# Kernel optimization log

Measured on AMD Instinct MI355X. Metric: run time of the kernel, lower is better.

Reference implementation:

```python
import jax, jax.numpy as jnp
import numpy as np
from math import lgamma

# dims (match init_kwargs / input_specs)
N_MELS = 80; MEM_DIM = 256; PRE1 = 256; PRE2 = 128
ATTN_LSTM = 256; ATTN_DIM = 128; S_FILT = 8; S_K = 21; D_FILT = 8; D_K = 21
P_LEN = 11; ALPHA = 0.1; BETA = 0.9; DEC_LSTM = 256; R = 2
B = 32; T_MELS = 400; T_ENC = 200


def _betabinom_prior():
    # beta-binomial pmf over [0, P_LEN-1] with n = P_LEN-1, a=ALPHA, b=BETA
    n = P_LEN - 1
    def pmf(k):
        return np.exp(lgamma(n + 1) - lgamma(k + 1) - lgamma(n - k + 1)
                      + lgamma(k + ALPHA) + lgamma(n - k + BETA) - lgamma(n + ALPHA + BETA)
                      - (lgamma(ALPHA) + lgamma(BETA) - lgamma(ALPHA + BETA)))
    return np.array([pmf(k) for k in range(P_LEN)], dtype=np.float32)


def setup_inputs() -> dict:
    ks = iter(jax.random.split(jax.random.key(0), 40))
    def w(*shape):
        return jax.random.normal(next(ks), shape, jnp.float32) / float(np.sqrt(shape[-1]))
    inp = {}
    inp["mels"] = jax.random.normal(next(ks), (B, N_MELS, T_MELS), jnp.float32)
    inp["memory"] = jax.random.normal(next(ks), (B, T_ENC, MEM_DIM), jnp.float32)
    # prenet
    inp["pre_W1"] = w(PRE1, N_MELS); inp["pre_b1"] = jnp.zeros((PRE1,), jnp.float32)
    inp["pre_W2"] = w(PRE2, PRE1); inp["pre_b2"] = jnp.zeros((PRE2,), jnp.float32)
    # attention LSTMCell (input = prenet[-1] + memory_dim)
    inp["al_Wih"] = w(4 * ATTN_LSTM, PRE2 + MEM_DIM); inp["al_Whh"] = w(4 * ATTN_LSTM, ATTN_LSTM)
    inp["al_bih"] = jnp.zeros((4 * ATTN_LSTM,), jnp.float32); inp["al_bhh"] = jnp.zeros((4 * ATTN_LSTM,), jnp.float32)
    # dynamic convolution attention
    inp["att_W"] = w(ATTN_DIM, ATTN_LSTM); inp["att_Wb"] = jnp.zeros((ATTN_DIM,), jnp.float32)
    inp["att_V"] = w(D_FILT * D_K, ATTN_DIM)
    inp["att_F"] = w(S_FILT, 1, S_K)
    inp["att_U"] = w(ATTN_DIM, S_FILT)
    inp["att_T"] = w(ATTN_DIM, D_FILT); inp["att_Tb"] = jnp.zeros((ATTN_DIM,), jnp.float32)
    inp["att_v"] = w(ATTN_DIM)
    inp["prior"] = jnp.asarray(_betabinom_prior())
    # decoder LSTMCell (input = attn_lstm_size + memory_dim)
    inp["dl_Wih"] = w(4 * DEC_LSTM, ATTN_LSTM + MEM_DIM); inp["dl_Whh"] = w(4 * DEC_LSTM, DEC_LSTM)
    inp["dl_bih"] = jnp.zeros((4 * DEC_LSTM,), jnp.float32); inp["dl_bhh"] = jnp.zeros((4 * DEC_LSTM,), jnp.float32)
    # acoustic projection
    inp["ac_W"] = w(N_MELS * R, DEC_LSTM + MEM_DIM); inp["ac_b"] = jnp.zeros((N_MELS * R,), jnp.float32)
    return inp


def _forward(mels, memory, pre_W1, pre_b1, pre_W2, pre_b2,
             al_Wih, al_Whh, al_bih, al_bhh,
             att_W, att_Wb, att_V, att_F, att_U, att_T, att_Tb, att_v, prior,
             dl_Wih, dl_Whh, dl_bih, dl_bhh, ac_W, ac_b):
    Bq = mels.shape[0]
    dn = ('NCH', 'OIH', 'NCH')
    prior_k = prior[::-1][None, None, :]  # torch registers flipped prior as conv kernel

    def lstm(x, h, c, Wih, Whh, bih, bhh):
        gates = x @ Wih.T + bih + h @ Whh.T + bhh
        i, f, g, o = jnp.split(gates, 4, axis=-1)
        c_new = jax.nn.sigmoid(f) * c + jax.nn.sigmoid(i) * jnp.tanh(g)
        return jax.nn.sigmoid(o) * jnp.tanh(c_new), c_new

    def dca(query, align):
        # query [B, attn_lstm], align [B, T_enc]
        T = align.shape[-1]
        # causal prior convolution, log-clamped
        p = jax.lax.conv_general_dilated(align[:, None, :], prior_k, (1,), [(P_LEN - 1, 0)], dimension_numbers=dn)[:, 0]
        p = jnp.log(jnp.clip(p, 1e-6))
        # per-example dynamic filters G: [B, C*K]
        G = jnp.tanh(query @ att_W.T + att_Wb) @ att_V.T
        g = jax.lax.conv_general_dilated(align[None, :, :], G.reshape(Bq * D_FILT, 1, D_K), (1,),
                                         [((D_K - 1) // 2,) * 2], dimension_numbers=dn,
                                         feature_group_count=Bq)[0].reshape(Bq, D_FILT, T)
        # static filters: [B, S, T]
        f = jax.lax.conv_general_dilated(align[:, None, :], att_F, (1,), [((S_K - 1) // 2,) * 2], dimension_numbers=dn)
        e = jnp.tanh(jnp.einsum('bst,as->bta', f, att_U) + jnp.einsum('bct,ac->bta', g, att_T) + att_Tb) @ att_v
        return jax.nn.softmax(e + p, axis=-1)

    def step(carry, x):
        align, ctx, h1, c1, h2, c2 = carry
        # prenet (dropout disabled: eval-mode deterministic reference)
        pre = jax.nn.relu(jax.nn.relu(x @ pre_W1.T + pre_b1) @ pre_W2.T + pre_b2)
        h1, c1 = lstm(jnp.concatenate([ctx, pre], -1), h1, c1, al_Wih, al_Whh, al_bih, al_bhh)
        align = dca(h1, align)
        ctx = jnp.einsum('bt,btd->bd', align, memory)
        h2, c2 = lstm(jnp.concatenate([h1, ctx], -1), h2, c2, dl_Wih, dl_Whh, dl_bih, dl_bhh)
        out = (jnp.concatenate([h2, ctx], -1) @ ac_W.T + ac_b).reshape(Bq, N_MELS, R)
        return (align, ctx, h1, c1, h2, c2), (out, align)

    T_enc = memory.shape[1]
    align0 = jnp.zeros((Bq, T_enc), jnp.float32).at[:, 0].set(1.0)  # one-hot at position 0
    carry0 = (align0,
              jnp.zeros((Bq, MEM_DIM), jnp.float32),
              jnp.zeros((Bq, ATTN_LSTM), jnp.float32), jnp.zeros((Bq, ATTN_LSTM), jnp.float32),
              jnp.zeros((Bq, DEC_LSTM), jnp.float32), jnp.zeros((Bq, DEC_LSTM), jnp.float32))
    # teacher forcing: step t>0 consumes ground-truth frame mels[:, :, t-1] for t in range(0, T, R)
    frames = jnp.moveaxis(mels[:, :, R - 1::R], 2, 0)  # [steps, B, N]
    xs = jnp.concatenate([jnp.zeros((1, Bq, N_MELS), jnp.float32), frames[:-1]], axis=0)
    _, (outs, aligns) = jax.lax.scan(step, carry0, xs)
    output_mels = jnp.moveaxis(outs, 0, 2).reshape(Bq, N_MELS, -1)  # cat along time: [B, N, T]
    alignments = jnp.moveaxis(aligns, 0, 2)  # stack dim=2: [B, T_enc, steps]
    return output_mels, alignments


def reference(mels, memory, pre_W1, pre_b1, pre_W2, pre_b2,
              al_Wih, al_Whh, al_bih, al_bhh,
              att_W, att_Wb, att_V, att_F, att_U, att_T, att_Tb, att_v, prior,
              dl_Wih, dl_Whh, dl_bih, dl_bhh, ac_W, ac_b):
    return _forward(mels, memory, pre_W1, pre_b1, pre_W2, pre_b2,
                    al_Wih, al_Whh, al_bih, al_bhh,
                    att_W, att_Wb, att_V, att_F, att_U, att_T, att_Tb, att_v, prior,
                    dl_Wih, dl_Whh, dl_bih, dl_bhh, ac_W, ac_b)
```

## Files before the change

kernel.cpp:

```cpp
#include <hip/hip_runtime.h>
#include <math.h>

#define BB 32
#define TENC 200
#define NMELS 80
#define TMELS 400
#define STEPS 200
#define MEM 256
#define PRE1N 256
#define PRE2N 128
#define AD 128
#define DK 21
#define DF 8
#define SK 21
#define SF 8
#define PL 11
#define BLK 1024

#define QW1 0u
#define QW2 655360u
#define HP5 1441792u
#define WS_ATTWT 761856u
#define WS_PW1T  816128u
#define WS_PW2T  836608u
#define WS_PRE2  869376u
#define WS_MEMH  1688576u
#define WS_AVTH  2507776u

#define L_XS   0
#define L_H1   768
#define L_C1   1024
#define L_H2   1280
#define L_C2   1536
#define L_CTX  1792
#define L_AL   2048
#define L_PS   2248
#define L_ES   2448
#define L_P4   2656
#define L_QS   6752
#define L_GS   6880
#define L_FS   7048
#define L_WF   8648
#define L_PR   8816
#define L_RB   8828
#define L_B1   8848
#define L_B2   9872
#define L_AW   10896
#define DYNF   27280
#define DYNB   (DYNF*4)

__device__ __forceinline__ float sigm(float x){ return 1.f/(1.f+__expf(-x)); }
__device__ __forceinline__ float tanh_fast(float x){
  float ax = fabsf(x);
  float z = __expf(-2.f*ax);
  float r = (1.f - z)/(1.f + z);
  return (x < 0.f) ? -r : r;
}
__device__ __forceinline__ unsigned short to_bf16(float f){
  unsigned u = __float_as_uint(f);
  return (unsigned short)((u + 0x7fffu + ((u>>16)&1u)) >> 16);
}

#define FMA8S(wv, xa, xb, acc) \
  acc += __uint_as_float((wv).x<<16)*(xa).x + __uint_as_float((wv).x&0xffff0000u)*(xa).y \
       + __uint_as_float((wv).y<<16)*(xa).z + __uint_as_float((wv).y&0xffff0000u)*(xa).w \
       + __uint_as_float((wv).z<<16)*(xb).x + __uint_as_float((wv).z&0xffff0000u)*(xb).y \
       + __uint_as_float((wv).w<<16)*(xb).z + __uint_as_float((wv).w&0xffff0000u)*(xb).w;

__global__ __launch_bounds__(256) void trk(const float* __restrict__ s, float* __restrict__ d, int R, int C){
  int i = blockIdx.x*256 + threadIdx.x;
  if (i < R*C){ int r = i / C, c = i - r*C; d[c*R + r] = s[i]; }
}
__global__ __launch_bounds__(256) void pkq1c(const float* __restrict__ wih, const float* __restrict__ whh,
                                             unsigned short* __restrict__ d){
  int i = blockIdx.x*256 + threadIdx.x;
  if (i < 1024*640){
    int c = i / 640, k = i - c*640;
    float v = (k < 384) ? wih[c*384 + k] : whh[c*256 + (k-384)];
    int q = k / 160, kr = k - 160*q, kk = kr >> 3, e = kr & 7;
    d[((unsigned)((q*20 + kk)*1024 + c))*8u + e] = to_bf16(v);
  }
}
__global__ __launch_bounds__(256) void pkq2c(const float* __restrict__ wih, const float* __restrict__ whh,
                                             unsigned short* __restrict__ d){
  int i = blockIdx.x*256 + threadIdx.x;
  if (i < 1024*768){
    int c = i / 768, k = i - c*768;
    float v = (k < 512) ? wih[c*512 + k] : whh[c*256 + (k-512)];
    int q = k / 192, kr = k - 192*q, kk = kr >> 3, e = kr & 7;
    d[((unsigned)((q*24 + kk)*1024 + c))*8u + e] = to_bf16(v);
  }
}
__global__ __launch_bounds__(256) void pk8h(const float* __restrict__ s, unsigned short* __restrict__ d, int R, int C){
  int i = blockIdx.x*256 + threadIdx.x;
  if (i < R*C){ int r = i / C, c = i - r*C; d[(unsigned)(c>>3)*(unsigned)R*8u + (unsigned)r*8u + (c&7)] = to_bf16(s[i]); }
}
__global__ __launch_bounds__(256) void pkmem(const float* __restrict__ s, unsigned short* __restrict__ d, int n){
  int i = blockIdx.x*256 + threadIdx.x;
  if (i < n) d[i] = to_bf16(s[i]);
}
__global__ __launch_bounds__(256) void pkavt(const float* __restrict__ s, unsigned short* __restrict__ d){
  int i = blockIdx.x*256 + threadIdx.x;
  if (i < 128*168){ int k = i/168, a = i - k*168; d[i] = to_bf16(s[a*128 + k]); }
}

__global__ __launch_bounds__(256) void prenetk(const float* __restrict__ mels,
    const float* __restrict__ b1, const float* __restrict__ b2, float* __restrict__ ws){
  int t = blockIdx.x, tid = threadIdx.x;
  __shared__ float xS[BB*NMELS];
  __shared__ float p1S[BB*PRE1N];
  const float* W1T = ws + WS_PW1T;
  const float* W2T = ws + WS_PW2T;
  for (int i=tid;i<BB*NMELS;i+=256){
    int r = i/NMELS, k = i - r*NMELS;
    xS[i] = (t==0)?0.f : mels[r*NMELS*TMELS + k*TMELS + (2*t-1)];
  }
  __syncthreads();
  {
    float acc[BB];
    #pragma unroll
    for (int r=0;r<BB;r++) acc[r]=0.f;
    for (int k=0;k<NMELS;k++){
      float w = W1T[k*PRE1N + tid];
      #pragma unroll
      for (int r=0;r<BB;r++) acc[r] += xS[r*NMELS+k]*w;
    }
    float bb = b1[tid];
    #pragma unroll
    for (int r=0;r<BB;r++) p1S[r*PRE1N+tid] = fmaxf(acc[r]+bb, 0.f);
  }
  __syncthreads();
  if (tid < PRE2N){
    float acc[BB];
    #pragma unroll
    for (int r=0;r<BB;r++) acc[r]=0.f;
    for (int k=0;k<PRE1N;k++){
      float w = W2T[k*PRE2N + tid];
      #pragma unroll
      for (int r=0;r<BB;r++) acc[r] += p1S[r*PRE1N+k]*w;
    }
    float bb = b2[tid];
    #pragma unroll
    for (int r=0;r<BB;r++) ws[WS_PRE2 + ((unsigned)t*BB + r)*PRE2N + tid] = fmaxf(acc[r]+bb, 0.f);
  }
}

__global__ __launch_bounds__(BLK) void decoder(
    const float* __restrict__ albih, const float* __restrict__ albhh,
    const float* __restrict__ dlbih, const float* __restrict__ dlbhh,
    const float* __restrict__ prior, const float* __restrict__ attF,
    const float* __restrict__ attWb, const float* __restrict__ attU,
    const float* __restrict__ attT, const float* __restrict__ attTb,
    const float* __restrict__ attv,
    const float* __restrict__ acb, const float* __restrict__ ws,
    float* __restrict__ out){
  extern __shared__ float sm[];
  const int b = blockIdx.x, tid = threadIdx.x;
  unsigned short* aWh = (unsigned short*)(sm + L_AW);
  const unsigned* aWu = (const unsigned*)(sm + L_AW);

  if (tid < 256){
    sm[L_H1+tid]=0.f; sm[L_C1+tid]=0.f; sm[L_H2+tid]=0.f; sm[L_C2+tid]=0.f; sm[L_CTX+tid]=0.f;
    sm[L_XS+tid]=0.f;
    sm[L_XS+384+tid]=0.f;
  }
  if (tid >= 256 && tid < 384) sm[L_XS+tid] = ws[WS_PRE2 + ((unsigned)0*BB + b)*PRE2N + (tid-256)];
  if (tid < TENC) sm[L_AL+tid] = (tid==0)?1.f:0.f;
  sm[L_B1+tid] = albih[tid] + albhh[tid];
  sm[L_B2+tid] = dlbih[tid] + dlbhh[tid];
  if (tid < SF*SK) sm[L_WF+tid] = attF[tid];
  if (tid < PL)    sm[L_PR+tid] = prior[tid];
  for (int i = tid; i < 32768; i += BLK) aWh[i] = to_bf16(ws[WS_ATTWT + i]);
  __syncthreads();

  const unsigned short* hw = (const unsigned short*)ws;
  const unsigned short* Q1 = hw + QW1;
  const unsigned short* Q2 = hw + QW2;
  const unsigned short* P5 = hw + HP5;
  const unsigned* memh = (const unsigned*)(ws + WS_MEMH);
  const unsigned short* avth = (const unsigned short*)(ws + WS_AVTH);
  const int q = tid >> 8, c0 = tid & 255;

  for (int t = 0; t < STEPS; ++t){
    {
      const float* xq = sm + L_XS + 160*q;
      const unsigned short* Wq = Q1 + (unsigned)q*163840u;
      float a0=0.f, a1=0.f, a2=0.f, a3=0.f;
      #pragma unroll 2
      for (int kk = 0; kk < 20; kk++){
        float4 xa = *(const float4*)(xq + 8*kk);
        float4 xb = *(const float4*)(xq + 8*kk + 4);
        const unsigned short* wr = Wq + (unsigned)kk*8192u + c0*8u;
        uint4 w0 = *(const uint4*)(wr);
        uint4 w1 = *(const uint4*)(wr + 2048);
        uint4 w2 = *(const uint4*)(wr + 4096);
        uint4 w3 = *(const uint4*)(wr + 6144);
        FMA8S(w0, xa, xb, a0)
        FMA8S(w1, xa, xb, a1)
        FMA8S(w2, xa, xb, a2)
        FMA8S(w3, xa, xb, a3)
      }
      sm[L_P4 + q*1024 + c0      ] = a0;
      sm[L_P4 + q*1024 + c0 + 256] = a1;
      sm[L_P4 + q*1024 + c0 + 512] = a2;
      sm[L_P4 + q*1024 + c0 + 768] = a3;
    }
    __syncthreads();
    if (tid < 256){
      float g[4];
      #pragma unroll
      for (int gg2 = 0; gg2 < 4; gg2++){
        int col = gg2*256 + tid;
        g[gg2] = sm[L_B1+col] + sm[L_P4+col] + sm[L_P4+1024+col] + sm[L_P4+2048+col] + sm[L_P4+3072+col];
      }
      float c = sigm(g[1])*sm[L_C1+tid] + sigm(g[0])*tanh_fast(g[2]);
      sm[L_C1+tid] = c;
      sm[L_H1+tid] = sigm(g[3])*tanh_fast(c);
    }
    __syncthreads();
    if (tid < 512){
      const int quarter = tid >> 7, a = tid & 127;
      const int sel = a & 1, au = a >> 1;
      float s = 0.f;
      for (int k = 64*quarter; k < 64*quarter+64; k++){
        unsigned u = aWu[k*64 + au];
        float wv = __uint_as_float(sel ? (u & 0xffff0000u) : (u << 16));
        s += sm[L_H1+k]*wv;
      }
      sm[L_P4 + tid] = s;
    } else if (tid < 512+TENC){
      const int pos = tid - 512;
      float s = 0.f;
      #pragma unroll
      for (int jj = 0; jj < PL; jj++){ int qq = pos - jj; if (qq >= 0) s += sm[L_PR+jj]*sm[L_AL+qq]; }
      sm[L_PS+pos] = __logf(fmaxf(s, 1e-6f));
      #pragma unroll
      for (int c = 0; c < SF; c++){
        float s2 = 0.f;
        #pragma unroll
        for (int k = 0; k < SK; k++){ int qq = pos + k - 10; if (qq>=0 && qq<TENC) s2 += sm[L_WF+c*SK+k]*sm[L_AL+qq]; }
        sm[L_FS + c*TENC + pos] = s2;
      }
    } else if (tid < 872){
      if (t >= 1){
        const int col = tid - 712;
        float a0=0.f, a1=0.f;
        #pragma unroll 2
        for (int kk = 0; kk < 64; kk += 2){
          const float* xp0 = (kk   < 32) ? (sm + L_H2 + 8*kk)     : (sm + L_CTX + 8*kk - 256);
          const float* xp1 = (kk+1 < 32) ? (sm + L_H2 + 8*(kk+1)) : (sm + L_CTX + 8*(kk+1) - 256);
          uint4 w0 = *(const uint4*)(P5 + (unsigned)(kk  )*1280u + col*8u);
          uint4 w1 = *(const uint4*)(P5 + (unsigned)(kk+1)*1280u + col*8u);
          FMA8S(w0, *(const float4*)xp0, *(const float4*)(xp0+4), a0)
          FMA8S(w1, *(const float4*)xp1, *(const float4*)(xp1+4), a1)
        }
        const int m = col >> 1, r = col & 1;
        out[(unsigned)b*NMELS*TMELS + m*TMELS + 2*(t-1) + r] = a0+a1 + acb[col];
      }
    }
    __syncthreads();
    if (tid < AD) sm[L_QS+tid] = tanh_fast(attWb[tid] + sm[L_P4+tid] + sm[L_P4+128+tid] + sm[L_P4+256+tid] + sm[L_P4+384+tid]);
    __syncthreads();
    if (tid < DF*DK){
      float a = 0.f;
      for (int k = 0; k < AD; k++) a += sm[L_QS+k]*__uint_as_float(((unsigned)avth[k*(DF*DK)+tid])<<16);
      sm[L_GS+tid] = a;
    }
    __syncthreads();
    if (tid < 4*TENC){
      const int pos = tid >> 2, qr = tid & 3;
      float g[DF];
      #pragma unroll
      for (int c=0;c<DF;c++){
        float s=0.f;
        #pragma unroll
        for (int k=0;k<DK;k++){
          int q2 = pos + k - 10;
          if (q2>=0 && q2<TENC) s += sm[L_AL+q2]*sm[L_GS+c*DK+k];
        }
        g[c]=s;
      }
      float fv[SF];
      #pragma unroll
      for (int s2=0;s2<SF;s2++) fv[s2] = sm[L_FS + s2*TENC + pos];
      float pp = 0.f;
      for (int h = qr*32; h < qr*32+32; h++){
        float u = attTb[h];
        #pragma unroll
        for (int s2=0;s2<SF;s2++) u += attU[h*SF+s2]*fv[s2];
        #pragma unroll
        for (int c=0;c<DF;c++) u += attT[h*DF+c]*g[c];
        pp += attv[h]*tanh_fast(u);
      }
      pp += __shfl_xor(pp,1);
      pp += __shfl_xor(pp,2);
      if (qr==0) sm[L_ES+pos] = pp + sm[L_PS+pos];
    }
    __syncthreads();
    if (tid < 64){
      float v0 = sm[L_ES+tid], v1 = sm[L_ES+64+tid], v2 = sm[L_ES+128+tid];
      float v3 = (tid < 8) ? sm[L_ES+192+tid] : -3.0e38f;
      float mx = fmaxf(fmaxf(v0,v1), fmaxf(v2,v3));
      for (int o=1;o<64;o<<=1) mx = fmaxf(mx, __shfl_xor(mx,o));
      float e0 = __expf(v0-mx), e1 = __expf(v1-mx), e2 = __expf(v2-mx);
      float e3 = (tid < 8) ? __expf(v3-mx) : 0.f;
      float sv = ((e0+e1)+(e2+e3));
      for (int o=1;o<64;o<<=1) sv += __shfl_xor(sv,o);
      float inv = 1.f/sv;
      float a0 = e0*inv, a1 = e1*inv, a2 = e2*inv;
      sm[L_AL+tid] = a0; sm[L_AL+64+tid] = a1; sm[L_AL+128+tid] = a2;
      unsigned ob = 1024000u + (unsigned)b*TENC*STEPS + (unsigned)t;
      out[ob + (unsigned)tid*STEPS]       = a0;
      out[ob + (unsigned)(64+tid)*STEPS]  = a1;
      out[ob + (unsigned)(128+tid)*STEPS] = a2;
      if (tid < 8){
        float a3 = e3*inv;
        sm[L_AL+192+tid] = a3;
        out[ob + (unsigned)(192+tid)*STEPS] = a3;
      }
    }
    __syncthreads();
    {
      const int grp2 = tid >> 7, jp = tid & 127;
      const unsigned base = ((unsigned)b*TENC)*128u + jp;
      float a0 = 0.f, a1 = 0.f;
      for (int p = grp2*25; p < grp2*25+25; p++){
        unsigned u = memh[base + (unsigned)p*128u];
        float al = sm[L_AL+p];
        a0 += al*__uint_as_float(u << 16);
        a1 += al*__uint_as_float(u & 0xffff0000u);
      }
      sm[L_P4 + grp2*256 + 2*jp    ] = a0;
      sm[L_P4 + grp2*256 + 2*jp + 1] = a1;
    }
    __syncthreads();
    if (tid < 256){
      float c = 0.f;
      #pragma unroll
      for (int g2 = 0; g2 < 8; g2++) c += sm[L_P4 + g2*256 + tid];
      sm[L_CTX+tid] = c;
      sm[L_XS+256+tid] = c;
    } else if (tid < 512){
      sm[L_XS + (tid-256)] = sm[L_H1 + (tid-256)];
    } else if (tid < 768){
      sm[L_XS + tid] = sm[L_H2 + (tid-512)];
    }
    __syncthreads();
    {
      const float* xq = sm + L_XS + 192*q;
      const unsigned short* Wq = Q2 + (unsigned)q*196608u;
      float a0=0.f, a1=0.f, a2=0.f, a3=0.f;
      #pragma unroll 2
      for (int kk = 0; kk < 24; kk++){
        float4 xa = *(const float4*)(xq + 8*kk);
        float4 xb = *(const float4*)(xq + 8*kk + 4);
        const unsigned short* wr = Wq + (unsigned)kk*8192u + c0*8u;
        uint4 w0 = *(const uint4*)(wr);
        uint4 w1 = *(const uint4*)(wr + 2048);
        uint4 w2 = *(const uint4*)(wr + 4096);
        uint4 w3 = *(const uint4*)(wr + 6144);
        FMA8S(w0, xa, xb, a0)
        FMA8S(w1, xa, xb, a1)
        FMA8S(w2, xa, xb, a2)
        FMA8S(w3, xa, xb, a3)
      }
      sm[L_P4 + q*1024 + c0      ] = a0;
      sm[L_P4 + q*1024 + c0 + 256] = a1;
      sm[L_P4 + q*1024 + c0 + 512] = a2;
      sm[L_P4 + q*1024 + c0 + 768] = a3;
    }
    __syncthreads();
    if (tid < 256){
      float g[4];
      #pragma unroll
      for (int gg2 = 0; gg2 < 4; gg2++){
        int col = gg2*256 + tid;
        g[gg2] = sm[L_B2+col] + sm[L_P4+col] + sm[L_P4+1024+col] + sm[L_P4+2048+col] + sm[L_P4+3072+col];
      }
      float c = sigm(g[1])*sm[L_C2+tid] + sigm(g[0])*tanh_fast(g[2]);
      sm[L_C2+tid] = c;
      sm[L_H2+tid] = sigm(g[3])*tanh_fast(c);
    } else if (tid < 384){
      if (t+1 < STEPS)
        sm[L_XS+tid] = __builtin_nontemporal_load(&ws[WS_PRE2 + ((unsigned)(t+1)*BB + b)*PRE2N + (tid-256)]);
    } else if (tid < 640){
      sm[L_XS+tid] = sm[L_H1 + (tid-384)];
    } else if (tid < 896){
      sm[L_XS + (tid-640)] = sm[L_CTX + (tid-640)];
    }
    __syncthreads();
  }
  if (tid < 160){
    const int col = tid;
    float a0=0.f, a1=0.f;
    #pragma unroll 2
    for (int kk = 0; kk < 64; kk += 2){
      const float* xp0 = (kk   < 32) ? (sm + L_H2 + 8*kk)     : (sm + L_CTX + 8*kk - 256);
      const float* xp1 = (kk+1 < 32) ? (sm + L_H2 + 8*(kk+1)) : (sm + L_CTX + 8*(kk+1) - 256);
      uint4 w0 = *(const uint4*)(P5 + (unsigned)(kk  )*1280u + col*8u);
      uint4 w1 = *(const uint4*)(P5 + (unsigned)(kk+1)*1280u + col*8u);
      FMA8S(w0, *(const float4*)xp0, *(const float4*)(xp0+4), a0)
      FMA8S(w1, *(const float4*)xp1, *(const float4*)(xp1+4), a1)
    }
    const int m = col >> 1, r = col & 1;
    out[(unsigned)b*NMELS*TMELS + m*TMELS + 2*(STEPS-1) + r] = a0+a1 + acb[col];
  }
}

extern "C" void kernel_launch(void* const* d_in, const int* in_sizes, int n_in,
                              void* d_out, int out_size, void* d_ws, size_t ws_size,
                              hipStream_t stream) {
  (void)in_sizes; (void)n_in; (void)out_size; (void)ws_size;
  const float* mels   = (const float*)d_in[0];
  const float* memory = (const float*)d_in[1];
  const float* pre_W1 = (const float*)d_in[2];
  const float* pre_b1 = (const float*)d_in[3];
  const float* pre_W2 = (const float*)d_in[4];
  const float* pre_b2 = (const float*)d_in[5];
  const float* al_Wih = (const float*)d_in[6];
  const float* al_Whh = (const float*)d_in[7];
  const float* al_bih = (const float*)d_in[8];
  const float* al_bhh = (const float*)d_in[9];
  const float* att_W  = (const float*)d_in[10];
  const float* att_Wb = (const float*)d_in[11];
  const float* att_V  = (const float*)d_in[12];
  const float* att_F  = (const float*)d_in[13];
  const float* att_U  = (const float*)d_in[14];
  const float* att_T  = (const float*)d_in[15];
  const float* att_Tb = (const float*)d_in[16];
  const float* att_v  = (const float*)d_in[17];
  const float* prior  = (const float*)d_in[18];
  const float* dl_Wih = (const float*)d_in[19];
  const float* dl_Whh = (const float*)d_in[20];
  const float* dl_bih = (const float*)d_in[21];
  const float* dl_bhh = (const float*)d_in[22];
  const float* ac_W   = (const float*)d_in[23];
  const float* ac_b   = (const float*)d_in[24];
  float* ws  = (float*)d_ws;
  unsigned short* hw = (unsigned short*)d_ws;
  float* out = (float*)d_out;

  hipFuncSetAttribute((const void*)decoder, hipFuncAttributeMaxDynamicSharedMemorySize, DYNB);

  auto TR = [&](const float* src, unsigned off, int R, int C){
    int n = R*C;
    trk<<<dim3((n+255)/256), dim3(256), 0, stream>>>(src, ws + off, R, C);
  };
  pkq1c<<<dim3((1024*640+255)/256), dim3(256), 0, stream>>>(al_Wih, al_Whh, hw + QW1);
  pkq2c<<<dim3((1024*768+255)/256), dim3(256), 0, stream>>>(dl_Wih, dl_Whh, hw + QW2);
  pk8h<<<dim3((160*512+255)/256), dim3(256), 0, stream>>>(ac_W, hw + HP5, 160, 512);
  TR(att_W,  WS_ATTWT, 128, 256);
  TR(pre_W1, WS_PW1T,  256, 80);
  TR(pre_W2, WS_PW2T,  128, 256);
  {
    int n = BB*TENC*MEM;
    pkmem<<<dim3((n+255)/256), dim3(256), 0, stream>>>(memory, (unsigned short*)(ws + WS_MEMH), n);
  }
  pkavt<<<dim3((128*168+255)/256), dim3(256), 0, stream>>>(att_V, (unsigned short*)(ws + WS_AVTH));

  prenetk<<<dim3(STEPS), dim3(256), 0, stream>>>(mels, pre_b1, pre_b2, ws);

  decoder<<<dim3(BB), dim3(BLK), DYNB, stream>>>(
      al_bih, al_bhh, dl_bih, dl_bhh, prior, att_F,
      att_Wb, att_U, att_T, att_Tb, att_v,
      ac_b, ws, out);
}
```

Measured before the change: 23.50 ms.

## Switch decoder weights and activations to fp16 with packed dot2 instructions

Converts all packed weights and memory from bf16 to fp16. LSTM inputs, hidden states and context are now kept in shared memory as fp16 vectors, so the matvecs use v_dot2_f32_f16 instead of unpacking bf16 and doing scalar FMAs. The attention W matrix is repacked into padded rows of half2 pairs so the query projection is also dot2-based. The aim is to cut ALU work and shared-memory traffic per step. In exchange, fp16 has less range than bf16, and the activations are now quantized as well as the weights.

```diff
diff --git a/kernel.cpp b/kernel.cpp
--- a/kernel.cpp
+++ b/kernel.cpp
@@ -27,27 +27,28 @@
 #define WS_MEMH  1688576u
 #define WS_AVTH  2507776u
 
-#define L_XS   0
-#define L_H1   768
-#define L_C1   1024
-#define L_H2   1280
-#define L_C2   1536
-#define L_CTX  1792
-#define L_AL   2048
-#define L_PS   2248
-#define L_ES   2448
-#define L_P4   2656
-#define L_QS   6752
-#define L_GS   6880
-#define L_FS   7048
-#define L_WF   8648
-#define L_PR   8816
-#define L_RB   8828
-#define L_B1   8848
-#define L_B2   9872
-#define L_AW   10896
-#define DYNF   27280
+#define L_C1   0
+#define L_C2   256
+#define L_AL   512
+#define L_PS   712
+#define L_ES   912
+#define L_QS   1120
+#define L_GS   1248
+#define L_WF   1416
+#define L_PR   1584
+#define L_B1   1600
+#define L_B2   2624
+#define L_FS   3648
+#define L_P4   5248
+#define L_AW   9344
+#define L_XB1  25856
+#define L_XB2  26240
+#define L_H1B  26624
+#define L_H2B  26752
+#define DYNF   26880
 #define DYNB   (DYNF*4)
+
+typedef _Float16 h2v __attribute__((ext_vector_type(2)));
 
 __device__ __forceinline__ float sigm(float x){ return 1.f/(1.f+__expf(-x)); }
 __device__ __forceinline__ float tanh_fast(float x){
@@ -56,16 +57,21 @@
   float r = (1.f - z)/(1.f + z);
   return (x < 0.f) ? -r : r;
 }
-__device__ __forceinline__ unsigned short to_bf16(float f){
-  unsigned u = __float_as_uint(f);
-  return (unsigned short)((u + 0x7fffu + ((u>>16)&1u)) >> 16);
-}
-
-#define FMA8S(wv, xa, xb, acc) \
-  acc += __uint_as_float((wv).x<<16)*(xa).x + __uint_as_float((wv).x&0xffff0000u)*(xa).y \
-       + __uint_as_float((wv).y<<16)*(xa).z + __uint_as_float((wv).y&0xffff0000u)*(xa).w \
-       + __uint_as_float((wv).z<<16)*(xb).x + __uint_as_float((wv).z&0xffff0000u)*(xb).y \
-       + __uint_as_float((wv).w<<16)*(xb).z + __uint_as_float((wv).w&0xffff0000u)*(xb).w;
+__device__ __forceinline__ unsigned short to_f16(float f){
+  _Float16 h = (_Float16)f;
+  return __builtin_bit_cast(unsigned short, h);
+}
+__device__ __forceinline__ float f16tof(unsigned short h){
+  return (float)__builtin_bit_cast(_Float16, h);
+}
+__device__ __forceinline__ float dot2(unsigned w, unsigned x, float acc){
+  return __builtin_amdgcn_fdot2(__builtin_bit_cast(h2v, w), __builtin_bit_cast(h2v, x), acc, false);
+}
+#define DOT8(wv, xv, acc) \
+  acc = dot2((wv).x, (xv).x, acc); \
+  acc = dot2((wv).y, (xv).y, acc); \
+  acc = dot2((wv).z, (xv).z, acc); \
+  acc = dot2((wv).w, (xv).w, acc);
 
 __global__ __launch_bounds__(256) void trk(const float* __restrict__ s, float* __restrict__ d, int R, int C){
   int i = blockIdx.x*256 + threadIdx.x;
@@ -78,7 +84,7 @@
     int c = i / 640, k = i - c*640;
     float v = (k < 384) ? wih[c*384 + k] : whh[c*256 + (k-384)];
     int q = k / 160, kr = k - 160*q, kk = kr >> 3, e = kr & 7;
-    d[((unsigned)((q*20 + kk)*1024 + c))*8u + e] = to_bf16(v);
+    d[((unsigned)((q*20 + kk)*1024 + c))*8u + e] = to_f16(v);
   }
 }
 __global__ __launch_bounds__(256) void pkq2c(const float* __restrict__ wih, const float* __restrict__ whh,
@@ -88,20 +94,20 @@
     int c = i / 768, k = i - c*768;
     float v = (k < 512) ? wih[c*512 + k] : whh[c*256 + (k-512)];
     int q = k / 192, kr = k - 192*q, kk = kr >> 3, e = kr & 7;
-    d[((unsigned)((q*24 + kk)*1024 + c))*8u + e] = to_bf16(v);
+    d[((unsigned)((q*24 + kk)*1024 + c))*8u + e] = to_f16(v);
   }
 }
 __global__ __launch_bounds__(256) void pk8h(const float* __restrict__ s, unsigned short* __restrict__ d, int R, int C){
   int i = blockIdx.x*256 + threadIdx.x;
-  if (i < R*C){ int r = i / C, c = i - r*C; d[(unsigned)(c>>3)*(unsigned)R*8u + (unsigned)r*8u + (c&7)] = to_bf16(s[i]); }
+  if (i < R*C){ int r = i / C, c = i - r*C; d[(unsigned)(c>>3)*(unsigned)R*8u + (unsigned)r*8u + (c&7)] = to_f16(s[i]); }
 }
 __global__ __launch_bounds__(256) void pkmem(const float* __restrict__ s, unsigned short* __restrict__ d, int n){
   int i = blockIdx.x*256 + threadIdx.x;
-  if (i < n) d[i] = to_bf16(s[i]);
+  if (i < n) d[i] = to_f16(s[i]);
 }
 __global__ __launch_bounds__(256) void pkavt(const float* __restrict__ s, unsigned short* __restrict__ d){
   int i = blockIdx.x*256 + threadIdx.x;
-  if (i < 128*168){ int k = i/168, a = i - k*168; d[i] = to_bf16(s[a*128 + k]); }
+  if (i < 128*168){ int k = i/168, a = i - k*168; d[i] = to_f16(s[a*128 + k]); }
 }
 
 __global__ __launch_bounds__(256) void prenetk(const float* __restrict__ mels,
@@ -156,21 +162,30 @@
     float* __restrict__ out){
   extern __shared__ float sm[];
   const int b = blockIdx.x, tid = threadIdx.x;
-  unsigned short* aWh = (unsigned short*)(sm + L_AW);
-  const unsigned* aWu = (const unsigned*)(sm + L_AW);
+  unsigned* aW2u = (unsigned*)(sm + L_AW);
+  unsigned short* xb1 = (unsigned short*)(sm + L_XB1);
+  unsigned short* xb2 = (unsigned short*)(sm + L_XB2);
+  unsigned short* h1b = (unsigned short*)(sm + L_H1B);
+  unsigned short* h2b = (unsigned short*)(sm + L_H2B);
+  const unsigned* h1p = (const unsigned*)(sm + L_H1B);
 
   if (tid < 256){
-    sm[L_H1+tid]=0.f; sm[L_C1+tid]=0.f; sm[L_H2+tid]=0.f; sm[L_C2+tid]=0.f; sm[L_CTX+tid]=0.f;
-    sm[L_XS+tid]=0.f;
-    sm[L_XS+384+tid]=0.f;
-  }
-  if (tid >= 256 && tid < 384) sm[L_XS+tid] = ws[WS_PRE2 + ((unsigned)0*BB + b)*PRE2N + (tid-256)];
+    sm[L_C1+tid]=0.f; sm[L_C2+tid]=0.f;
+    xb1[tid]=0; xb1[384+tid]=0;
+    h2b[tid]=0;
+  }
+  if (tid >= 256 && tid < 384) xb1[tid] = to_f16(ws[WS_PRE2 + (unsigned)b*PRE2N + (tid-256)]);
   if (tid < TENC) sm[L_AL+tid] = (tid==0)?1.f:0.f;
   sm[L_B1+tid] = albih[tid] + albhh[tid];
   sm[L_B2+tid] = dlbih[tid] + dlbhh[tid];
   if (tid < SF*SK) sm[L_WF+tid] = attF[tid];
   if (tid < PL)    sm[L_PR+tid] = prior[tid];
-  for (int i = tid; i < 32768; i += BLK) aWh[i] = to_bf16(ws[WS_ATTWT + i]);
+  for (int i = tid; i < 16384; i += BLK){
+    int a = i >> 7, kk = i & 127;
+    unsigned lo = to_f16(ws[WS_ATTWT + (unsigned)(2*kk)*128u + a]);
+    unsigned hi = to_f16(ws[WS_ATTWT + (unsigned)(2*kk+1)*128u + a]);
+    aW2u[a*129 + kk] = lo | (hi << 16);
+  }
   __syncthreads();
 
   const unsigned short* hw = (const unsigned short*)ws;
@@ -183,22 +198,21 @@
 
   for (int t = 0; t < STEPS; ++t){
     {
-      const float* xq = sm + L_XS + 160*q;
+      const uint4* xq = (const uint4*)(xb1 + 160*q);
       const unsigned short* Wq = Q1 + (unsigned)q*163840u;
       float a0=0.f, a1=0.f, a2=0.f, a3=0.f;
       #pragma unroll 2
       for (int kk = 0; kk < 20; kk++){
-        float4 xa = *(const float4*)(xq + 8*kk);
-        float4 xb = *(const float4*)(xq + 8*kk + 4);
+        uint4 xv = xq[kk];
         const unsigned short* wr = Wq + (unsigned)kk*8192u + c0*8u;
         uint4 w0 = *(const uint4*)(wr);
         uint4 w1 = *(const uint4*)(wr + 2048);
         uint4 w2 = *(const uint4*)(wr + 4096);
         uint4 w3 = *(const uint4*)(wr + 6144);
-        FMA8S(w0, xa, xb, a0)
-        FMA8S(w1, xa, xb, a1)
-        FMA8S(w2, xa, xb, a2)
-        FMA8S(w3, xa, xb, a3)
+        DOT8(w0, xv, a0)
+        DOT8(w1, xv, a1)
+        DOT8(w2, xv, a2)
+        DOT8(w3, xv, a3)
       }
       sm[L_P4 + q*1024 + c0      ] = a0;
       sm[L_P4 + q*1024 + c0 + 256] = a1;
@@ -215,18 +229,16 @@
       }
       float c = sigm(g[1])*sm[L_C1+tid] + sigm(g[0])*tanh_fast(g[2]);
       sm[L_C1+tid] = c;
-      sm[L_H1+tid] = sigm(g[3])*tanh_fast(c);
+      h1b[tid] = to_f16(sigm(g[3])*tanh_fast(c));
     }
     __syncthreads();
     if (tid < 512){
       const int quarter = tid >> 7, a = tid & 127;
-      const int sel = a & 1, au = a >> 1;
+      const unsigned* wrow = aW2u + a*129;
       float s = 0.f;
-      for (int k = 64*quarter; k < 64*quarter+64; k++){
-        unsigned u = aWu[k*64 + au];
-        float wv = __uint_as_float(sel ? (u & 0xffff0000u) : (u << 16));
-        s += sm[L_H1+k]*wv;
-      }
+      #pragma unroll 4
+      for (int kk = 32*quarter; kk < 32*quarter+32; kk++)
+        s = dot2(wrow[kk], h1p[kk], s);
       sm[L_P4 + tid] = s;
     } else if (tid < 512+TENC){
       const int pos = tid - 512;
@@ -244,15 +256,17 @@
     } else if (tid < 872){
       if (t >= 1){
         const int col = tid - 712;
+        const uint4* xv2  = (const uint4*)xb2;
+        const uint4* h2v4 = (const uint4*)h2b;
         float a0=0.f, a1=0.f;
         #pragma unroll 2
         for (int kk = 0; kk < 64; kk += 2){
-          const float* xp0 = (kk   < 32) ? (sm + L_H2 + 8*kk)     : (sm + L_CTX + 8*kk - 256);
-          const float* xp1 = (kk+1 < 32) ? (sm + L_H2 + 8*(kk+1)) : (sm + L_CTX + 8*(kk+1) - 256);
+          uint4 x0 = (kk   < 32) ? h2v4[kk]   : xv2[kk];
+          uint4 x1 = (kk+1 < 32) ? h2v4[kk+1] : xv2[kk+1];
           uint4 w0 = *(const uint4*)(P5 + (unsigned)(kk  )*1280u + col*8u);
           uint4 w1 = *(const uint4*)(P5 + (unsigned)(kk+1)*1280u + col*8u);
-          FMA8S(w0, *(const float4*)xp0, *(const float4*)(xp0+4), a0)
-          FMA8S(w1, *(const float4*)xp1, *(const float4*)(xp1+4), a1)
+          DOT8(w0, x0, a0)
+          DOT8(w1, x1, a1)
         }
         const int m = col >> 1, r = col & 1;
         out[(unsigned)b*NMELS*TMELS + m*TMELS + 2*(t-1) + r] = a0+a1 + acb[col];
@@ -263,7 +277,7 @@
     __syncthreads();
     if (tid < DF*DK){
       float a = 0.f;
-      for (int k = 0; k < AD; k++) a += sm[L_QS+k]*__uint_as_float(((unsigned)avth[k*(DF*DK)+tid])<<16);
+      for (int k = 0; k < AD; k++) a += sm[L_QS+k]*f16tof(avth[k*(DF*DK)+tid]);
       sm[L_GS+tid] = a;
     }
     __syncthreads();
@@ -327,8 +341,8 @@
       for (int p = grp2*25; p < grp2*25+25; p++){
         unsigned u = memh[base + (unsigned)p*128u];
         float al = sm[L_AL+p];
-        a0 += al*__uint_as_float(u << 16);
-        a1 += al*__uint_as_float(u & 0xffff0000u);
+        a0 += al*f16tof((unsigned short)(u & 0xffffu));
+        a1 += al*f16tof((unsigned short)(u >> 16));
       }
       sm[L_P4 + grp2*256 + 2*jp    ] = a0;
       sm[L_P4 + grp2*256 + 2*jp + 1] = a1;
@@ -338,31 +352,29 @@
       float c = 0.f;
       #pragma unroll
       for (int g2 = 0; g2 < 8; g2++) c += sm[L_P4 + g2*256 + tid];
-      sm[L_CTX+tid] = c;
-      sm[L_XS+256+tid] = c;
+      xb2[256+tid] = to_f16(c);
     } else if (tid < 512){
-      sm[L_XS + (tid-256)] = sm[L_H1 + (tid-256)];
+      xb2[tid-256] = h1b[tid-256];
     } else if (tid < 768){
-      sm[L_XS + tid] = sm[L_H2 + (tid-512)];
+      xb2[512 + (tid-512)] = h2b[tid-512];
     }
     __syncthreads();
     {
-      const float* xq = sm + L_XS + 192*q;
+      const uint4* xq = (const uint4*)(xb2 + 192*q);
       const unsigned short* Wq = Q2 + (unsigned)q*196608u;
       float a0=0.f, a1=0.f, a2=0.f, a3=0.f;
       #pragma unroll 2
       for (int kk = 0; kk < 24; kk++){
-        float4 xa = *(const float4*)(xq + 8*kk);
-        float4 xb = *(const float4*)(xq + 8*kk + 4);
+        uint4 xv = xq[kk];
         const unsigned short* wr = Wq + (unsigned)kk*8192u + c0*8u;
         uint4 w0 = *(const uint4*)(wr);
         uint4 w1 = *(const uint4*)(wr + 2048);
         uint4 w2 = *(const uint4*)(wr + 4096);
         uint4 w3 = *(const uint4*)(wr + 6144);
-        FMA8S(w0, xa, xb, a0)
-        FMA8S(w1, xa, xb, a1)
-        FMA8S(w2, xa, xb, a2)
-        FMA8S(w3, xa, xb, a3)
+        DOT8(w0, xv, a0)
+        DOT8(w1, xv, a1)
+        DOT8(w2, xv, a2)
+        DOT8(w3, xv, a3)
       }
       sm[L_P4 + q*1024 + c0      ] = a0;
       sm[L_P4 + q*1024 + c0 + 256] = a1;
@@ -379,28 +391,30 @@
       }
       float c = sigm(g[1])*sm[L_C2+tid] + sigm(g[0])*tanh_fast(g[2]);
       sm[L_C2+tid] = c;
-      sm[L_H2+tid] = sigm(g[3])*tanh_fast(c);
+      h2b[tid] = to_f16(sigm(g[3])*tanh_fast(c));
     } else if (tid < 384){
       if (t+1 < STEPS)
-        sm[L_XS+tid] = __builtin_nontemporal_load(&ws[WS_PRE2 + ((unsigned)(t+1)*BB + b)*PRE2N + (tid-256)]);
+        xb1[tid] = to_f16(__builtin_nontemporal_load(&ws[WS_PRE2 + ((unsigned)(t+1)*BB + b)*PRE2N + (tid-256)]));
     } else if (tid < 640){
-      sm[L_XS+tid] = sm[L_H1 + (tid-384)];
+      xb1[tid] = xb2[tid-384];
     } else if (tid < 896){
-      sm[L_XS + (tid-640)] = sm[L_CTX + (tid-640)];
+      xb1[tid-640] = xb2[256 + (tid-640)];
     }
     __syncthreads();
   }
   if (tid < 160){
     const int col = tid;
+    const uint4* xv2  = (const uint4*)xb2;
+    const uint4* h2v4 = (const uint4*)h2b;
     float a0=0.f, a1=0.f;
     #pragma unroll 2
     for (int kk = 0; kk < 64; kk += 2){
-      const float* xp0 = (kk   < 32) ? (sm + L_H2 + 8*kk)     : (sm + L_CTX + 8*kk - 256);
-      const float* xp1 = (kk+1 < 32) ? (sm + L_H2 + 8*(kk+1)) : (sm + L_CTX + 8*(kk+1) - 256);
+      uint4 x0 = (kk   < 32) ? h2v4[kk]   : xv2[kk];
+      uint4 x1 = (kk+1 < 32) ? h2v4[kk+1] : xv2[kk+1];
       uint4 w0 = *(const uint4*)(P5 + (unsigned)(kk  )*1280u + col*8u);
       uint4 w1 = *(const uint4*)(P5 + (unsigned)(kk+1)*1280u + col*8u);
-      FMA8S(w0, *(const float4*)xp0, *(const float4*)(xp0+4), a0)
-      FMA8S(w1, *(const float4*)xp1, *(const float4*)(xp1+4), a1)
+      DOT8(w0, x0, a0)
+      DOT8(w1, x1, a1)
     }
     const int m = col >> 1, r = col & 1;
     out[(unsigned)b*NMELS*TMELS + m*TMELS + 2*(STEPS-1) + r] = a0+a1 + acb[col];
```

After: 21.06 ms. -10.4%, faster.
